# Optimization experiments

Measured on AMD Instinct MI355X. Metric: run time of the kernel, lower is better.

Reference implementation:

```python
import jax, jax.numpy as jnp
import numpy as np

B, N, D = 2, 2048, 1024
H = 16
HS = D // H
EPS = 1e-6


def layer_norm(x, scale, bias):
    mu = jnp.mean(x, axis=-1, keepdims=True)
    var = jnp.mean(jnp.square(x - mu), axis=-1, keepdims=True)
    return (x - mu) * jax.lax.rsqrt(var + EPS) * scale + bias


def setup_inputs() -> dict:
    key = jax.random.key(0)
    ks = jax.random.split(key, 8)
    lecun = lambda k, shape: jax.random.normal(k, shape, jnp.float32) / jnp.sqrt(shape[0])
    return {
        "x": jax.random.normal(ks[0], (B, N, D), jnp.float32),
        "ln1_scale": jnp.ones((D,), jnp.float32),
        "ln1_bias": jnp.zeros((D,), jnp.float32),
        "w_qkv": lecun(ks[1], (D, 3 * D)),
        "w_out": lecun(ks[2], (D, D)),
        "b_out": jnp.zeros((D,), jnp.float32),
        "ln2_scale": jnp.ones((D,), jnp.float32),
        "ln2_bias": jnp.zeros((D,), jnp.float32),
        "w1": lecun(ks[3], (D, 2 * D)),
        "b1": jnp.zeros((2 * D,), jnp.float32),
        "w2": lecun(ks[4], (2 * D, D)),
        "b2": jnp.zeros((D,), jnp.float32),
    }


def reference(x, ln1_scale, ln1_bias, w_qkv, w_out, b_out,
              ln2_scale, ln2_bias, w1, b1, w2, b2):
    b, n, d = x.shape
    # --- attention sub-block ---
    xn = layer_norm(x, ln1_scale, ln1_bias)
    qkv = xn @ w_qkv                      # [B,N,3D]
    q, k, v = jnp.split(qkv, 3, axis=-1)
    q = q.reshape(b, n, H, HS)
    k = k.reshape(b, n, H, HS)
    v = v.reshape(b, n, H, HS)
    scores = jnp.einsum('bihd,bjhd->bhij', q, k) / jnp.sqrt(jnp.float32(HS))
    causal = jnp.tril(jnp.ones((n, n), bool))[None, None]
    scores = jnp.where(causal, scores, -jnp.inf)
    attn = jax.nn.softmax(scores, axis=-1)
    out_heads = jnp.einsum('bhij,bjhd->bihd', attn, v).reshape(b, n, d)
    x = x + out_heads @ w_out + b_out
    xn2 = layer_norm(x, ln2_scale, ln2_bias)
    y = jax.nn.gelu(xn2 @ w1 + b1)        # flax nn.gelu default approximate=True
    x = x + (y @ w2 + b2)
    return x
```

## Files before the change

kernel.cpp:

```cpp
#include <hip/hip_runtime.h>

#define D_MODEL 1024
#define NSEQ    2048
#define NBATCH  2
#define NHEAD   16
#define HSZ     64
#define MROWS   4096

typedef short s8v  __attribute__((ext_vector_type(8)));
typedef float f32x4 __attribute__((ext_vector_type(4)));

#define AS1(p) ((__attribute__((address_space(1))) const void*)(p))
#define AS3(p) ((__attribute__((address_space(3))) void*)(p))

__device__ __forceinline__ float b2f(unsigned short s) {
    union { unsigned u; float f; } z; z.u = (unsigned)s << 16; return z.f;
}
__device__ __forceinline__ unsigned short f2b(float f) {
    union { float f; unsigned u; } z; z.f = f;
    unsigned r = z.u + 0x7fffu + ((z.u >> 16) & 1u);
    return (unsigned short)(r >> 16);
}
__device__ __forceinline__ unsigned short f2b_trunc(float f) {
    union { float f; unsigned u; } z; z.f = f;
    return (unsigned short)(z.u >> 16);
}
__device__ __forceinline__ float gelu_f(float x) {
    float u = 0.7978845608028654f * (x + 0.044715f * x * x * x);
    float t = 1.f - 2.f / (1.f + __expf(2.f * u));
    return 0.5f * x * (1.f + t);
}

__global__ __launch_bounds__(256) void sniff_k(const unsigned short* __restrict__ xr,
                                               int* __restrict__ flag) {
    __shared__ int cnt[4];
    int tid = threadIdx.x, ok = 0;
    for (int i = tid; i < 2048; i += 256) {
        unsigned short u = xr[i];
        int e = (u >> 7) & 0xFF;
        if (u == 0 || (e >= 110 && e <= 135)) ok++;
    }
    #pragma unroll
    for (int off = 32; off; off >>= 1) ok += __shfl_down(ok, off);
    if ((tid & 63) == 0) cnt[tid >> 6] = ok;
    __syncthreads();
    if (tid == 0) {
        int tot = cnt[0] + cnt[1] + cnt[2] + cnt[3];
        *flag = (tot > 1843) ? 1 : 0;
    }
}

__global__ __launch_bounds__(256) void cvt_small_k(
    const void* p0, const void* p1, const void* p2, const void* p3,
    const void* p4, const void* p5, const void* p6,
    unsigned short* __restrict__ out, const int* __restrict__ flag)
{
    int i = blockIdx.x * 256 + threadIdx.x;
    const void* src; int off;
    if      (i < 1024) { src = p0; off = i; }
    else if (i < 2048) { src = p1; off = i - 1024; }
    else if (i < 3072) { src = p2; off = i - 2048; }
    else if (i < 4096) { src = p3; off = i - 3072; }
    else if (i < 5120) { src = p4; off = i - 4096; }
    else if (i < 7168) { src = p5; off = i - 5120; }
    else               { src = p6; off = i - 7168; }
    out[i] = (*flag) ? ((const unsigned short*)src)[off]
                     : f2b(((const float*)src)[off]);
}

__global__ __launch_bounds__(256) void transpose_all_k(
    const void* wqkv, const void* wout, const void* w1, const void* w2,
    unsigned short* t_qkv, unsigned short* t_out,
    unsigned short* t_w1, unsigned short* t_w2, const int* __restrict__ flag)
{
    __shared__ unsigned short t[32][33];
    int bid = blockIdx.x;
    const void* W; unsigned short* Wt; int K, N, bx, by;
    if      (bid < 3072) { W = wqkv; Wt = t_qkv; K = 1024; N = 3072; bx = bid % 96; by = bid / 96; }
    else if (bid < 4096) { bid -= 3072; W = wout; Wt = t_out; K = 1024; N = 1024; bx = bid % 32; by = bid / 32; }
    else if (bid < 6144) { bid -= 4096; W = w1;   Wt = t_w1;  K = 1024; N = 2048; bx = bid % 64; by = bid / 64; }
    else                 { bid -= 6144; W = w2;   Wt = t_w2;  K = 2048; N = 1024; bx = bid % 32; by = bid / 32; }
    int f = *flag;
    int n0 = bx * 32, k0 = by * 32;
    int x = threadIdx.x & 31, y = threadIdx.x >> 5;
    #pragma unroll
    for (int r = 0; r < 32; r += 8) {
        size_t idx = (size_t)(k0 + r + y) * N + n0 + x;
        t[r + y][x] = f ? ((const unsigned short*)W)[idx]
                        : f2b(((const float*)W)[idx]);
    }
    __syncthreads();
    #pragma unroll
    for (int r = 0; r < 32; r += 8)
        Wt[(size_t)(n0 + r + y) * K + k0 + x] = t[x][r + y];
}

__global__ __launch_bounds__(256) void ln1f_k(
    const void* __restrict__ x_raw, const unsigned short* __restrict__ scale,
    const unsigned short* __restrict__ bias, unsigned short* __restrict__ xb,
    unsigned short* __restrict__ xn, const int* __restrict__ flag)
{
    int row = blockIdx.x, tid = threadIdx.x;
    int f = *flag;
    float v[4], s = 0.f, s2 = 0.f;
    #pragma unroll
    for (int i = 0; i < 4; ++i) {
        size_t idx = (size_t)row * D_MODEL + tid + i * 256;
        float t = f ? b2f(((const unsigned short*)x_raw)[idx])
                    : ((const float*)x_raw)[idx];
        v[i] = t; s += t; s2 += t * t;
    }
    #pragma unroll
    for (int off = 32; off; off >>= 1) { s += __shfl_down(s, off); s2 += __shfl_down(s2, off); }
    __shared__ float rs[4], rs2[4];
    int w = tid >> 6;
    if ((tid & 63) == 0) { rs[w] = s; rs2[w] = s2; }
    __syncthreads();
    float S  = rs[0] + rs[1] + rs[2] + rs[3];
    float S2 = rs2[0] + rs2[1] + rs2[2] + rs2[3];
    float mean = S * (1.f / D_MODEL);
    float var  = S2 * (1.f / D_MODEL) - mean * mean;
    float rstd = rsqrtf(var + 1e-6f);
    #pragma unroll
    for (int i = 0; i < 4; ++i) {
        int d = tid + i * 256;
        size_t idx = (size_t)row * D_MODEL + d;
        xb[idx] = f2b(v[i]);
        xn[idx] = f2b((v[i] - mean) * rstd * b2f(scale[d]) + b2f(bias[d]));
    }
}

__global__ __launch_bounds__(256) void ln_k(
    const unsigned short* __restrict__ x, const unsigned short* __restrict__ scale,
    const unsigned short* __restrict__ bias, unsigned short* __restrict__ out)
{
    int row = blockIdx.x, tid = threadIdx.x;
    const unsigned short* xr = x + (size_t)row * D_MODEL;
    float v[4], s = 0.f, s2 = 0.f;
    #pragma unroll
    for (int i = 0; i < 4; ++i) {
        float t = b2f(xr[tid + i * 256]);
        v[i] = t; s += t; s2 += t * t;
    }
    #pragma unroll
    for (int off = 32; off; off >>= 1) { s += __shfl_down(s, off); s2 += __shfl_down(s2, off); }
    __shared__ float rs[4], rs2[4];
    int w = tid >> 6;
    if ((tid & 63) == 0) { rs[w] = s; rs2[w] = s2; }
    __syncthreads();
    float S  = rs[0] + rs[1] + rs[2] + rs[3];
    float S2 = rs2[0] + rs2[1] + rs2[2] + rs2[3];
    float mean = S * (1.f / D_MODEL);
    float var  = S2 * (1.f / D_MODEL) - mean * mean;
    float rstd = rsqrtf(var + 1e-6f);
    #pragma unroll
    for (int i = 0; i < 4; ++i) {
        int d = tid + i * 256;
        out[(size_t)row * D_MODEL + d] =
            f2b((v[i] - mean) * rstd * b2f(scale[d]) + b2f(bias[d]));
    }
}

template<int TN, int ACT, int RES, int ODYN>
__global__ __launch_bounds__(256) void gemm128_k(
    const unsigned short* __restrict__ A, const unsigned short* __restrict__ Bt,
    const unsigned short* __restrict__ bias, const unsigned short* __restrict__ resid,
    void* __restrict__ Cp, int M, int Nn, int K, const int* __restrict__ flag)
{
    constexpr int MT = (TN == 128) ? 4 : 2;
    __shared__ short As[128 * 64];
    __shared__ short Bs[TN * 64];
    int tid = threadIdx.x;
    int m0 = blockIdx.y * 128, n0 = blockIdx.x * TN;
    int lane = tid & 63, w = tid >> 6;
    int a_base = (TN == 128) ? (w >> 1) * 64 : w * 32;
    int b_base = (TN == 128) ? (w & 1) * 64 : 0;
    int mm = lane & 15, q = lane >> 4;

    f32x4 zero = {0.f, 0.f, 0.f, 0.f};
    f32x4 acc[MT][4];
    #pragma unroll
    for (int mt = 0; mt < MT; ++mt)
        #pragma unroll
        for (int nt = 0; nt < 4; ++nt) acc[mt][nt] = zero;

    int grow   = lane >> 3;
    int gchunk = ((lane & 7) ^ grow) * 8;
    const unsigned short* Ab = A  + (size_t)(m0 + w * 32 + grow) * K + gchunk;
    const unsigned short* Bb = Bt + (size_t)(n0 + w * (TN / 4) + grow) * K + gchunk;
    int swz = (mm & 7);

    for (int k0 = 0; k0 < K; k0 += 64) {
        __syncthreads();
        #pragma unroll
        for (int s = 0; s < 4; ++s)
            __builtin_amdgcn_global_load_lds(AS1(Ab + k0 + (size_t)(s * 8) * K),
                                             AS3(&As[(w * 32 + s * 8) * 64]), 16, 0, 0);
        #pragma unroll
        for (int s = 0; s < TN / 32; ++s)
            __builtin_amdgcn_global_load_lds(AS1(Bb + k0 + (size_t)(s * 8) * K),
                                             AS3(&Bs[(w * (TN / 4) + s * 8) * 64]), 16, 0, 0);
        __syncthreads();
        #pragma unroll
        for (int kk = 0; kk < 2; ++kk) {
            int col = ((kk * 4 + q) ^ swz) * 8;
            s8v af[MT], bf[4];
            #pragma unroll
            for (int mt = 0; mt < MT; ++mt)
                af[mt] = *(const s8v*)&As[(a_base + mt * 16 + mm) * 64 + col];
            #pragma unroll
            for (int nt = 0; nt < 4; ++nt)
                bf[nt] = *(const s8v*)&Bs[(b_base + nt * 16 + mm) * 64 + col];
            #pragma unroll
            for (int mt = 0; mt < MT; ++mt)
                #pragma unroll
                for (int nt = 0; nt < 4; ++nt)
                    acc[mt][nt] = __builtin_amdgcn_mfma_f32_16x16x32_bf16(
                        af[mt], bf[nt], acc[mt][nt], 0, 0, 0);
        }
    }

    int f = ODYN ? *flag : 1;
    #pragma unroll
    for (int nt = 0; nt < 4; ++nt) {
        int gc = n0 + b_base + nt * 16 + mm;
        float bv = bias ? b2f(bias[gc]) : 0.f;
        #pragma unroll
        for (int mt = 0; mt < MT; ++mt) {
            #pragma unroll
            for (int r = 0; r < 4; ++r) {
                int gr = m0 + a_base + mt * 16 + q * 4 + r;
                float v = acc[mt][nt][r] + bv;
                if (ACT == 1) v = gelu_f(v);
                if (RES == 1) v += b2f(resid[(size_t)gr * Nn + gc]);
                if (f) ((unsigned short*)Cp)[(size_t)gr * Nn + gc] = f2b(v);
                else   ((float*)Cp)[(size_t)gr * Nn + gc] = v;
            }
        }
    }
}

__global__ __launch_bounds__(256, 3) void fattn_k(
    const unsigned short* __restrict__ qkv, unsigned short* __restrict__ attn_out)
{
    int bh = blockIdx.x;
    int h = bh & (NHEAD - 1), b = bh >> 4;
    int qt = gridDim.y - 1 - blockIdx.y;
    int q0 = qt * 64;
    size_t base = (size_t)b * NSEQ * (3 * D_MODEL);

    __shared__ __align__(16) short Ks[128][72];
    __shared__ __align__(16) short Vts[64][136];
    __shared__ __align__(16) short Ps[64][136];

    int tid = threadIdx.x, lane = tid & 63, w = tid >> 6;
    int mm = lane & 15, q = lane >> 4;

    s8v qf[2];
    #pragma unroll
    for (int kk = 0; kk < 2; ++kk)
        qf[kk] = *(const s8v*)(qkv + base + (size_t)(q0 + w * 16 + mm) * (3 * D_MODEL)
                               + h * HSZ + kk * 32 + q * 8);

    f32x4 zero = {0.f, 0.f, 0.f, 0.f};
    f32x4 acc_o[4] = {zero, zero, zero, zero};
    float l_acc[4] = {0.f, 0.f, 0.f, 0.f};

    int kr = tid >> 1;
    int kc = (tid & 1) * 32;
    int kp = tid >> 3;
    int vd = (tid & 7) * 8;

    const unsigned short* kbase = qkv + base + D_MODEL + h * HSZ;
    const unsigned short* vbase = qkv + base + 2 * D_MODEL + h * HSZ;

    int nstages = (qt + 2) >> 1;

    s8v kv0, kv1, kv2, kv3, vv0, vv1, vv2, vv3;
    {
        const unsigned short* kb = kbase;
        const unsigned short* vb = vbase;
        kv0 = *(const s8v*)(kb + (size_t)kr * (3 * D_MODEL) + kc);
        kv1 = *(const s8v*)(kb + (size_t)kr * (3 * D_MODEL) + kc + 8);
        kv2 = *(const s8v*)(kb + (size_t)kr * (3 * D_MODEL) + kc + 16);
        kv3 = *(const s8v*)(kb + (size_t)kr * (3 * D_MODEL) + kc + 24);
        vv0 = *(const s8v*)(vb + (size_t)(2 * kp)      * (3 * D_MODEL) + vd);
        vv1 = *(const s8v*)(vb + (size_t)(2 * kp + 1)  * (3 * D_MODEL) + vd);
        vv2 = *(const s8v*)(vb + (size_t)(2 * kp + 64) * (3 * D_MODEL) + vd);
        vv3 = *(const s8v*)(vb + (size_t)(2 * kp + 65) * (3 * D_MODEL) + vd);
    }

    for (int t = 0; t < nstages; ++t) {
        int j0 = t * 128;
        int nsub = (j0 < q0) ? 2 : 1;

        __syncthreads();
        *(s8v*)&Ks[kr][kc]      = kv0;
        *(s8v*)&Ks[kr][kc + 8]  = kv1;
        *(s8v*)&Ks[kr][kc + 16] = kv2;
        *(s8v*)&Ks[kr][kc + 24] = kv3;
        int c0 = (2 * kp + vd) & 63;
        #pragma unroll
        for (int e = 0; e < 8; ++e) {
            unsigned p0 = (unsigned)(unsigned short)vv0[e] |
                          ((unsigned)(unsigned short)vv1[e] << 16);
            unsigned p1 = (unsigned)(unsigned short)vv2[e] |
                          ((unsigned)(unsigned short)vv3[e] << 16);
            *(unsigned*)&Vts[vd + e][c0]      = p0;
            *(unsigned*)&Vts[vd + e][64 + c0] = p1;
        }
        if (t + 1 < nstages) {
            const unsigned short* kb = kbase + (size_t)(j0 + 128) * (3 * D_MODEL);
            const unsigned short* vb = vbase + (size_t)(j0 + 128) * (3 * D_MODEL);
            kv0 = *(const s8v*)(kb + (size_t)kr * (3 * D_MODEL) + kc);
            kv1 = *(const s8v*)(kb + (size_t)kr * (3 * D_MODEL) + kc + 8);
            kv2 = *(const s8v*)(kb + (size_t)kr * (3 * D_MODEL) + kc + 16);
            kv3 = *(const s8v*)(kb + (size_t)kr * (3 * D_MODEL) + kc + 24);
            vv0 = *(const s8v*)(vb + (size_t)(2 * kp)      * (3 * D_MODEL) + vd);
            vv1 = *(const s8v*)(vb + (size_t)(2 * kp + 1)  * (3 * D_MODEL) + vd);
            vv2 = *(const s8v*)(vb + (size_t)(2 * kp + 64) * (3 * D_MODEL) + vd);
            vv3 = *(const s8v*)(vb + (size_t)(2 * kp + 65) * (3 * D_MODEL) + vd);
        }
        __syncthreads();

        f32x4 sc[8];
        #pragma unroll
        for (int i = 0; i < 8; ++i) sc[i] = zero;
        #pragma unroll
        for (int sub = 0; sub < 2; ++sub) {
            if (sub >= nsub) break;
            #pragma unroll
            for (int kk = 0; kk < 2; ++kk) {
                #pragma unroll
                for (int nt = 0; nt < 4; ++nt) {
                    s8v bv = *(const s8v*)&Ks[sub * 64 + nt * 16 + mm][kk * 32 + q * 8];
                    sc[sub * 4 + nt] = __builtin_amdgcn_mfma_f32_16x16x32_bf16(
                        qf[kk], bv, sc[sub * 4 + nt], 0, 0, 0);
                }
            }
        }

        int pswz = 16 * q;
        #pragma unroll
        for (int sub = 0; sub < 2; ++sub) {
            if (sub >= nsub) break;
            bool need_mask = (j0 + sub * 64 + 63) > (q0 + w * 16);
            #pragma unroll
            for (int nt = 0; nt < 4; ++nt) {
                int gj = j0 + sub * 64 + nt * 16 + mm;
                #pragma unroll
                for (int r = 0; r < 4; ++r) {
                    float p = __expf(sc[sub * 4 + nt][r] * 0.125f);
                    if (need_mask && gj > (q0 + w * 16 + q * 4 + r)) p = 0.f;
                    l_acc[r] += p;
                    Ps[w * 16 + q * 4 + r][sub * 64 + ((nt * 16 + mm + pswz) & 63)] =
                        (short)f2b_trunc(p);
                }
            }
        }

        int rq16 = 16 * ((mm >> 2) & 3);
        #pragma unroll
        for (int kk4 = 0; kk4 < 4; ++kk4) {
            if (kk4 >= nsub * 2) break;
            int sub = kk4 >> 1, kkl = kk4 & 1;
            s8v av = *(const s8v*)&Ps[w * 16 + mm]
                        [sub * 64 + ((kkl * 32 + q * 8 + rq16) & 63)];
            #pragma unroll
            for (int nt = 0; nt < 4; ++nt) {
                int d = nt * 16 + mm;
                int c = sub * 64 + ((kkl * 32 + q * 8 + (d & 56)) & 63);
                s8v bv = *(const s8v*)&Vts[d][c];
                acc_o[nt] = __builtin_amdgcn_mfma_f32_16x16x32_bf16(av, bv, acc_o[nt], 0, 0, 0);
            }
        }
    }

    #pragma unroll
    for (int r = 0; r < 4; ++r) {
        #pragma unroll
        for (int msk = 1; msk < 16; msk <<= 1) l_acc[r] += __shfl_xor(l_acc[r], msk);
        l_acc[r] = 1.f / l_acc[r];
    }
    #pragma unroll
    for (int nt = 0; nt < 4; ++nt) {
        int d = nt * 16 + mm;
        #pragma unroll
        for (int r = 0; r < 4; ++r) {
            int row = q0 + w * 16 + q * 4 + r;
            attn_out[(size_t)(b * NSEQ + row) * D_MODEL + h * HSZ + d] =
                f2b(acc_o[nt][r] * l_acc[r]);
        }
    }
}

extern "C" void kernel_launch(void* const* d_in, const int* in_sizes, int n_in,
                              void* d_out, int out_size, void* d_ws, size_t ws_size,
                              hipStream_t stream)
{
    const void* x_raw  = d_in[0];
    const void* ln1s_r = d_in[1];
    const void* ln1b_r = d_in[2];
    const void* wqkv_r = d_in[3];
    const void* wout_r = d_in[4];
    const void* bout_r = d_in[5];
    const void* ln2s_r = d_in[6];
    const void* ln2b_r = d_in[7];
    const void* w1_r   = d_in[8];
    const void* b1_r   = d_in[9];
    const void* w2_r   = d_in[10];
    const void* b2_r   = d_in[11];

    char* ws = (char*)d_ws;
    const size_t MB = 1024 * 1024;
    unsigned short* wt_qkv = (unsigned short*)(ws + 0 * MB);
    unsigned short* wt_out = (unsigned short*)(ws + 6 * MB);
    unsigned short* wt_w1  = (unsigned short*)(ws + 8 * MB);
    unsigned short* wt_w2  = (unsigned short*)(ws + 12 * MB);
    unsigned short* xb     = (unsigned short*)(ws + 16 * MB);
    unsigned short* xn     = (unsigned short*)(ws + 24 * MB);
    unsigned short* qkvb   = (unsigned short*)(ws + 32 * MB);
    unsigned short* x1     = (unsigned short*)(ws + 48 * MB);
    int*            flag   = (int*)           (ws + 56 * MB);
    unsigned short* cbias  = (unsigned short*)(ws + 56 * MB + 1024);
    unsigned short* attnb  = xn;
    unsigned short* xn2    = xn;
    unsigned short* hb     = qkvb;

    unsigned short* c_ln1s = cbias + 0;
    unsigned short* c_ln1b = cbias + 1024;
    unsigned short* c_bout = cbias + 2048;
    unsigned short* c_ln2s = cbias + 3072;
    unsigned short* c_ln2b = cbias + 4096;
    unsigned short* c_b1   = cbias + 5120;
    unsigned short* c_b2   = cbias + 7168;

    sniff_k<<<1, 256, 0, stream>>>((const unsigned short*)x_raw, flag);
    cvt_small_k<<<32, 256, 0, stream>>>(ln1s_r, ln1b_r, bout_r, ln2s_r, ln2b_r,
                                        b1_r, b2_r, cbias, flag);
    transpose_all_k<<<8192, 256, 0, stream>>>(wqkv_r, wout_r, w1_r, w2_r,
                                              wt_qkv, wt_out, wt_w1, wt_w2, flag);
    ln1f_k<<<MROWS, 256, 0, stream>>>(x_raw, c_ln1s, c_ln1b, xb, xn, flag);
    gemm128_k<128, 0, 0, 0><<<dim3(24, 32), 256, 0, stream>>>(
        xn, wt_qkv, nullptr, nullptr, qkvb, MROWS, 3072, 1024, flag);
    fattn_k<<<dim3(NBATCH * NHEAD, NSEQ / 64), 256, 0, stream>>>(qkvb, attnb);
    gemm128_k<64, 0, 1, 0><<<dim3(16, 32), 256, 0, stream>>>(
        attnb, wt_out, c_bout, xb, x1, MROWS, 1024, 1024, flag);
    ln_k<<<MROWS, 256, 0, stream>>>(x1, c_ln2s, c_ln2b, xn2);
    gemm128_k<128, 1, 0, 0><<<dim3(16, 32), 256, 0, stream>>>(
        xn2, wt_w1, c_b1, nullptr, hb, MROWS, 2048, 1024, flag);
    gemm128_k<64, 0, 1, 1><<<dim3(16, 32), 256, 0, stream>>>(
        hb, wt_w2, c_b2, x1, d_out, MROWS, 1024, 2048, flag);
}
```

Before: 285.4 us.

## Stage GEMM epilogue through LDS for vectorized stores; fold softmax scale and row-sum into MFMA

Measured after the change: 287.9 us. About the same (+0.9%).

```diff
diff --git a/kernel.cpp b/kernel.cpp
--- a/kernel.cpp
+++ b/kernel.cpp
@@ -168,8 +168,13 @@
     void* __restrict__ Cp, int M, int Nn, int K, const int* __restrict__ flag)
 {
     constexpr int MT = (TN == 128) ? 4 : 2;
-    __shared__ short As[128 * 64];
-    __shared__ short Bs[TN * 64];
+    constexpr int SW = TN + 4;
+    constexpr int STAGE = 128 * 64 + TN * 64;
+    constexpr int EPI   = 128 * SW;
+    constexpr int SMEMN = (STAGE > EPI) ? STAGE : EPI;
+    __shared__ short smem[SMEMN];
+    short* As = smem;
+    short* Bs = smem + 128 * 64;
     int tid = threadIdx.x;
     int m0 = blockIdx.y * 128, n0 = blockIdx.x * TN;
     int lane = tid & 63, w = tid >> 6;
@@ -220,22 +225,52 @@
         }
     }
 
+    __syncthreads();
+    #pragma unroll
+    for (int nt = 0; nt < 4; ++nt)
+        #pragma unroll
+        for (int mt = 0; mt < MT; ++mt)
+            #pragma unroll
+            for (int r = 0; r < 4; ++r)
+                smem[(a_base + mt * 16 + q * 4 + r) * SW + b_base + nt * 16 + mm] =
+                    (short)f2b(acc[mt][nt][r]);
+    __syncthreads();
+
+    constexpr int LPR = TN / 8;
+    constexpr int RPP = 256 / LPR;
+    int erow = tid / LPR;
+    int ecol = (tid % LPR) * 8;
     int f = ODYN ? *flag : 1;
-    #pragma unroll
-    for (int nt = 0; nt < 4; ++nt) {
-        int gc = n0 + b_base + nt * 16 + mm;
-        float bv = bias ? b2f(bias[gc]) : 0.f;
-        #pragma unroll
-        for (int mt = 0; mt < MT; ++mt) {
-            #pragma unroll
-            for (int r = 0; r < 4; ++r) {
-                int gr = m0 + a_base + mt * 16 + q * 4 + r;
-                float v = acc[mt][nt][r] + bv;
-                if (ACT == 1) v = gelu_f(v);
-                if (RES == 1) v += b2f(resid[(size_t)gr * Nn + gc]);
-                if (f) ((unsigned short*)Cp)[(size_t)gr * Nn + gc] = f2b(v);
-                else   ((float*)Cp)[(size_t)gr * Nn + gc] = v;
-            }
+    float bias8[8];
+    #pragma unroll
+    for (int e = 0; e < 8; ++e) bias8[e] = bias ? b2f(bias[n0 + ecol + e]) : 0.f;
+
+    #pragma unroll
+    for (int p = 0; p < 128 / RPP; ++p) {
+        int row = p * RPP + erow;
+        int gr = m0 + row;
+        s8v vv = *(const s8v*)&smem[row * SW + ecol];
+        float vf[8];
+        #pragma unroll
+        for (int e = 0; e < 8; ++e) {
+            vf[e] = b2f((unsigned short)vv[e]) + bias8[e];
+            if (ACT == 1) vf[e] = gelu_f(vf[e]);
+        }
+        if (RES == 1) {
+            s8v rv = *(const s8v*)(resid + (size_t)gr * Nn + n0 + ecol);
+            #pragma unroll
+            for (int e = 0; e < 8; ++e) vf[e] += b2f((unsigned short)rv[e]);
+        }
+        if (f) {
+            s8v ov;
+            #pragma unroll
+            for (int e = 0; e < 8; ++e) ov[e] = (short)f2b(vf[e]);
+            *(s8v*)&((unsigned short*)Cp)[(size_t)gr * Nn + n0 + ecol] = ov;
+        } else {
+            f32x4 o0 = {vf[0], vf[1], vf[2], vf[3]};
+            f32x4 o1 = {vf[4], vf[5], vf[6], vf[7]};
+            *(f32x4*)&((float*)Cp)[(size_t)gr * Nn + n0 + ecol] = o0;
+            *(f32x4*)&((float*)Cp)[(size_t)gr * Nn + n0 + ecol + 4] = o1;
         }
     }
 }
@@ -258,13 +293,19 @@
 
     s8v qf[2];
     #pragma unroll
-    for (int kk = 0; kk < 2; ++kk)
-        qf[kk] = *(const s8v*)(qkv + base + (size_t)(q0 + w * 16 + mm) * (3 * D_MODEL)
-                               + h * HSZ + kk * 32 + q * 8);
+    for (int kk = 0; kk < 2; ++kk) {
+        s8v t = *(const s8v*)(qkv + base + (size_t)(q0 + w * 16 + mm) * (3 * D_MODEL)
+                              + h * HSZ + kk * 32 + q * 8);
+        #pragma unroll
+        for (int e = 0; e < 8; ++e)
+            t[e] = (short)f2b_trunc(b2f((unsigned short)t[e]) * 0.125f);
+        qf[kk] = t;
+    }
 
     f32x4 zero = {0.f, 0.f, 0.f, 0.f};
     f32x4 acc_o[4] = {zero, zero, zero, zero};
-    float l_acc[4] = {0.f, 0.f, 0.f, 0.f};
+    f32x4 acc_l = zero;
+    const s8v ones = {0x3F80, 0x3F80, 0x3F80, 0x3F80, 0x3F80, 0x3F80, 0x3F80, 0x3F80};
 
     int kr = tid >> 1;
     int kc = (tid & 1) * 32;
@@ -350,9 +391,8 @@
                 int gj = j0 + sub * 64 + nt * 16 + mm;
                 #pragma unroll
                 for (int r = 0; r < 4; ++r) {
-                    float p = __expf(sc[sub * 4 + nt][r] * 0.125f);
+                    float p = __expf(sc[sub * 4 + nt][r]);
                     if (need_mask && gj > (q0 + w * 16 + q * 4 + r)) p = 0.f;
-                    l_acc[r] += p;
                     Ps[w * 16 + q * 4 + r][sub * 64 + ((nt * 16 + mm + pswz) & 63)] =
                         (short)f2b_trunc(p);
                 }
@@ -373,15 +413,13 @@
                 s8v bv = *(const s8v*)&Vts[d][c];
                 acc_o[nt] = __builtin_amdgcn_mfma_f32_16x16x32_bf16(av, bv, acc_o[nt], 0, 0, 0);
             }
-        }
-    }
-
-    #pragma unroll
-    for (int r = 0; r < 4; ++r) {
-        #pragma unroll
-        for (int msk = 1; msk < 16; msk <<= 1) l_acc[r] += __shfl_xor(l_acc[r], msk);
-        l_acc[r] = 1.f / l_acc[r];
-    }
+            acc_l = __builtin_amdgcn_mfma_f32_16x16x32_bf16(av, ones, acc_l, 0, 0, 0);
+        }
+    }
+
+    float linv[4];
+    #pragma unroll
+    for (int r = 0; r < 4; ++r) linv[r] = 1.f / acc_l[r];
     #pragma unroll
     for (int nt = 0; nt < 4; ++nt) {
         int d = nt * 16 + mm;
@@ -389,7 +427,7 @@
         for (int r = 0; r < 4; ++r) {
             int row = q0 + w * 16 + q * 4 + r;
             attn_out[(size_t)(b * NSEQ + row) * D_MODEL + h * HSZ + d] =
-                f2b(acc_o[nt][r] * l_acc[r]);
+                f2b(acc_o[nt][r] * linv[r]);
         }
     }
 }
```

## Double query tile per attention block and compute row sums via MFMA

Applied to the files above, without the earlier changes.

After: 298.4 us. 4.5% more time.

```diff
diff --git a/kernel.cpp b/kernel.cpp
--- a/kernel.cpp
+++ b/kernel.cpp
@@ -240,31 +240,44 @@
     }
 }
 
-__global__ __launch_bounds__(256, 3) void fattn_k(
+__global__ __launch_bounds__(256, 2) void fattn_k(
     const unsigned short* __restrict__ qkv, unsigned short* __restrict__ attn_out)
 {
     int bh = blockIdx.x;
     int h = bh & (NHEAD - 1), b = bh >> 4;
     int qt = gridDim.y - 1 - blockIdx.y;
-    int q0 = qt * 64;
+    int q0 = qt * 128;
     size_t base = (size_t)b * NSEQ * (3 * D_MODEL);
 
     __shared__ __align__(16) short Ks[128][72];
     __shared__ __align__(16) short Vts[64][136];
-    __shared__ __align__(16) short Ps[64][136];
+    __shared__ __align__(16) short Ps[128][136];
 
     int tid = threadIdx.x, lane = tid & 63, w = tid >> 6;
     int mm = lane & 15, q = lane >> 4;
-
-    s8v qf[2];
-    #pragma unroll
-    for (int kk = 0; kk < 2; ++kk)
-        qf[kk] = *(const s8v*)(qkv + base + (size_t)(q0 + w * 16 + mm) * (3 * D_MODEL)
-                               + h * HSZ + kk * 32 + q * 8);
+    int wq0 = q0 + w * 32;
+
+    s8v qf[2][2];
+    #pragma unroll
+    for (int s = 0; s < 2; ++s)
+        #pragma unroll
+        for (int kk = 0; kk < 2; ++kk) {
+            s8v t = *(const s8v*)(qkv + base + (size_t)(wq0 + s * 16 + mm) * (3 * D_MODEL)
+                                  + h * HSZ + kk * 32 + q * 8);
+            #pragma unroll
+            for (int e = 0; e < 8; ++e)
+                t[e] = (short)f2b_trunc(b2f((unsigned short)t[e]) * 0.125f);
+            qf[s][kk] = t;
+        }
 
     f32x4 zero = {0.f, 0.f, 0.f, 0.f};
-    f32x4 acc_o[4] = {zero, zero, zero, zero};
-    float l_acc[4] = {0.f, 0.f, 0.f, 0.f};
+    f32x4 acc_o[2][4];
+    #pragma unroll
+    for (int s = 0; s < 2; ++s)
+        #pragma unroll
+        for (int nt = 0; nt < 4; ++nt) acc_o[s][nt] = zero;
+    f32x4 acc_l[2] = {zero, zero};
+    const s8v ones = {0x3F80, 0x3F80, 0x3F80, 0x3F80, 0x3F80, 0x3F80, 0x3F80, 0x3F80};
 
     int kr = tid >> 1;
     int kc = (tid & 1) * 32;
@@ -274,7 +287,7 @@
     const unsigned short* kbase = qkv + base + D_MODEL + h * HSZ;
     const unsigned short* vbase = qkv + base + 2 * D_MODEL + h * HSZ;
 
-    int nstages = (qt + 2) >> 1;
+    int nstages = qt + 1;
 
     s8v kv0, kv1, kv2, kv3, vv0, vv1, vv2, vv3;
     {
@@ -292,7 +305,6 @@
 
     for (int t = 0; t < nstages; ++t) {
         int j0 = t * 128;
-        int nsub = (j0 < q0) ? 2 : 1;
 
         __syncthreads();
         *(s8v*)&Ks[kr][kc]      = kv0;
@@ -323,38 +335,39 @@
         }
         __syncthreads();
 
-        f32x4 sc[8];
-        #pragma unroll
-        for (int i = 0; i < 8; ++i) sc[i] = zero;
+        int nsub = (wq0 + 31 >= j0 + 64) ? 2 : 1;
+        int pswz = 16 * q;
+
         #pragma unroll
         for (int sub = 0; sub < 2; ++sub) {
             if (sub >= nsub) break;
-            #pragma unroll
-            for (int kk = 0; kk < 2; ++kk) {
+            f32x4 sc[2][4];
+            #pragma unroll
+            for (int s = 0; s < 2; ++s)
+                #pragma unroll
+                for (int nt = 0; nt < 4; ++nt) sc[s][nt] = zero;
+            #pragma unroll
+            for (int kk = 0; kk < 2; ++kk)
                 #pragma unroll
                 for (int nt = 0; nt < 4; ++nt) {
                     s8v bv = *(const s8v*)&Ks[sub * 64 + nt * 16 + mm][kk * 32 + q * 8];
-                    sc[sub * 4 + nt] = __builtin_amdgcn_mfma_f32_16x16x32_bf16(
-                        qf[kk], bv, sc[sub * 4 + nt], 0, 0, 0);
+                    sc[0][nt] = __builtin_amdgcn_mfma_f32_16x16x32_bf16(qf[0][kk], bv, sc[0][nt], 0, 0, 0);
+                    sc[1][nt] = __builtin_amdgcn_mfma_f32_16x16x32_bf16(qf[1][kk], bv, sc[1][nt], 0, 0, 0);
                 }
-            }
-        }
-
-        int pswz = 16 * q;
-        #pragma unroll
-        for (int sub = 0; sub < 2; ++sub) {
-            if (sub >= nsub) break;
-            bool need_mask = (j0 + sub * 64 + 63) > (q0 + w * 16);
-            #pragma unroll
-            for (int nt = 0; nt < 4; ++nt) {
-                int gj = j0 + sub * 64 + nt * 16 + mm;
+            #pragma unroll
+            for (int s = 0; s < 2; ++s) {
+                int qb = wq0 + s * 16;
+                bool need_mask = (j0 + sub * 64 + 63) > qb;
                 #pragma unroll
-                for (int r = 0; r < 4; ++r) {
-                    float p = __expf(sc[sub * 4 + nt][r] * 0.125f);
-                    if (need_mask && gj > (q0 + w * 16 + q * 4 + r)) p = 0.f;
-                    l_acc[r] += p;
-                    Ps[w * 16 + q * 4 + r][sub * 64 + ((nt * 16 + mm + pswz) & 63)] =
-                        (short)f2b_trunc(p);
+                for (int nt = 0; nt < 4; ++nt) {
+                    int gj = j0 + sub * 64 + nt * 16 + mm;
+                    #pragma unroll
+                    for (int r = 0; r < 4; ++r) {
+                        float p = __expf(sc[s][nt][r]);
+                        if (need_mask && gj > qb + q * 4 + r) p = 0.f;
+                        Ps[w * 32 + s * 16 + q * 4 + r][sub * 64 + ((nt * 16 + mm + pswz) & 63)] =
+                            (short)f2b_trunc(p);
+                    }
                 }
             }
         }
@@ -364,32 +377,38 @@
         for (int kk4 = 0; kk4 < 4; ++kk4) {
             if (kk4 >= nsub * 2) break;
             int sub = kk4 >> 1, kkl = kk4 & 1;
-            s8v av = *(const s8v*)&Ps[w * 16 + mm]
-                        [sub * 64 + ((kkl * 32 + q * 8 + rq16) & 63)];
+            s8v bv[4];
             #pragma unroll
             for (int nt = 0; nt < 4; ++nt) {
                 int d = nt * 16 + mm;
-                int c = sub * 64 + ((kkl * 32 + q * 8 + (d & 56)) & 63);
-                s8v bv = *(const s8v*)&Vts[d][c];
-                acc_o[nt] = __builtin_amdgcn_mfma_f32_16x16x32_bf16(av, bv, acc_o[nt], 0, 0, 0);
+                bv[nt] = *(const s8v*)&Vts[d][sub * 64 + ((kkl * 32 + q * 8 + (d & 56)) & 63)];
             }
-        }
-    }
-
-    #pragma unroll
-    for (int r = 0; r < 4; ++r) {
-        #pragma unroll
-        for (int msk = 1; msk < 16; msk <<= 1) l_acc[r] += __shfl_xor(l_acc[r], msk);
-        l_acc[r] = 1.f / l_acc[r];
-    }
-    #pragma unroll
-    for (int nt = 0; nt < 4; ++nt) {
-        int d = nt * 16 + mm;
-        #pragma unroll
-        for (int r = 0; r < 4; ++r) {
-            int row = q0 + w * 16 + q * 4 + r;
-            attn_out[(size_t)(b * NSEQ + row) * D_MODEL + h * HSZ + d] =
-                f2b(acc_o[nt][r] * l_acc[r]);
+            #pragma unroll
+            for (int s = 0; s < 2; ++s) {
+                s8v av = *(const s8v*)&Ps[w * 32 + s * 16 + mm]
+                            [sub * 64 + ((kkl * 32 + q * 8 + rq16) & 63)];
+                #pragma unroll
+                for (int nt = 0; nt < 4; ++nt)
+                    acc_o[s][nt] = __builtin_amdgcn_mfma_f32_16x16x32_bf16(av, bv[nt], acc_o[s][nt], 0, 0, 0);
+                acc_l[s] = __builtin_amdgcn_mfma_f32_16x16x32_bf16(av, ones, acc_l[s], 0, 0, 0);
+            }
+        }
+    }
+
+    #pragma unroll
+    for (int s = 0; s < 2; ++s) {
+        float linv[4];
+        #pragma unroll
+        for (int r = 0; r < 4; ++r) linv[r] = 1.f / acc_l[s][r];
+        #pragma unroll
+        for (int nt = 0; nt < 4; ++nt) {
+            int d = nt * 16 + mm;
+            #pragma unroll
+            for (int r = 0; r < 4; ++r) {
+                int row = wq0 + s * 16 + q * 4 + r;
+                attn_out[(size_t)(b * NSEQ + row) * D_MODEL + h * HSZ + d] =
+                    f2b(acc_o[s][nt][r] * linv[r]);
+            }
         }
     }
 }
@@ -443,7 +462,7 @@
     ln1f_k<<<MROWS, 256, 0, stream>>>(x_raw, c_ln1s, c_ln1b, xb, xn, flag);
     gemm128_k<128, 0, 0, 0><<<dim3(24, 32), 256, 0, stream>>>(
         xn, wt_qkv, nullptr, nullptr, qkvb, MROWS, 3072, 1024, flag);
-    fattn_k<<<dim3(NBATCH * NHEAD, NSEQ / 64), 256, 0, stream>>>(qkvb, attnb);
+    fattn_k<<<dim3(NBATCH * NHEAD, NSEQ / 128), 256, 0, stream>>>(qkvb, attnb);
     gemm128_k<64, 0, 1, 0><<<dim3(16, 32), 256, 0, stream>>>(
         attnb, wt_out, c_bout, xb, x1, MROWS, 1024, 1024, flag);
     ln_k<<<MROWS, 256, 0, stream>>>(x1, c_ln2s, c_ln2b, xn2);
```
